# Kernel optimization log

Hardware: AMD Instinct MI355X
Metric: run time of the kernel (lower is better)

Reference implementation:

```python
import jax, jax.numpy as jnp
import numpy as np

NEG_SLOPE = 0.01  # torch nn.LeakyReLU default


def setup_inputs() -> dict:
    key = jax.random.key(0)
    kq, kk, kv, km, kw = jax.random.split(key, 5)
    B, Lq, Lk, Dk, Dv = 4, 2048, 2048, 512, 512
    q = jax.random.normal(kq, (B, Lq, Dk), dtype=jnp.float32)
    k = jax.random.normal(kk, (B, Lk, Dk), dtype=jnp.float32)
    v = jax.random.normal(kv, (B, Lk, Dv), dtype=jnp.float32)
    attn_mask = jax.random.randint(km, (B, Lq, Lk), 0, 2).astype(jnp.int32)
    # xavier_normal for (Dk, 1): std = sqrt(2 / (Dk + 1))
    weight = jax.random.normal(kw, (Dk, 1), dtype=jnp.float32) * np.sqrt(2.0 / (Dk + 1))
    return {"q": q, "k": k, "v": v, "attn_mask": attn_mask, "weight": weight}


def reference(q, k, v, attn_mask, weight):
    # (q - k) @ w  ==  (q @ w) - (k @ w): avoid the [B,Lq,Lk,Dk] intermediate.
    qw = jnp.einsum('bqd,do->bq', q, weight)  # [B, Lq]
    kw = jnp.einsum('bkd,do->bk', k, weight)  # [B, Lk]
    scores = qw[:, :, None] - kw[:, None, :]  # [B, Lq, Lk]
    attn = jnp.where(scores >= 0, scores, NEG_SLOPE * scores)  # LeakyReLU
    masked = attn_mask == 0
    attn = jnp.where(masked, -jnp.inf, attn)
    attn = jax.nn.softmax(attn, axis=2)
    attn = jnp.where(masked, 0.0, attn)
    # dropout omitted (eval mode / identity for reference correctness)
    output = jnp.einsum('bqk,bkd->bqd', attn, v)  # bmm
    return output, attn
```

## Files before the change

### kernel.cpp

```cpp
#include <hip/hip_runtime.h>
#include <math.h>

#define BB 4
#define LQ 2048
#define LK 2048
#define DK 512
#define DV 512

typedef __attribute__((ext_vector_type(8))) _Float16 f16x8;
typedef __attribute__((ext_vector_type(2))) _Float16 f16x2;
typedef __attribute__((ext_vector_type(4))) float f32x4;

#define WS_QW    0
#define WS_KW    8192
#define WS_M     16384
#define WS_INV   24576
#define WS_VF16  32768
#define NOUT     ((size_t)BB * LQ * DV)

__device__ __forceinline__ void lds_barrier() {
    __builtin_amdgcn_sched_barrier(0);
    asm volatile("s_waitcnt lgkmcnt(0)\n\ts_barrier" ::: "memory");
    __builtin_amdgcn_sched_barrier(0);
}

__global__ __launch_bounds__(256) void qkw_kernel(const float* __restrict__ q,
                                                  const float* __restrict__ k,
                                                  const float* __restrict__ w,
                                                  float* __restrict__ ws) {
    int gw   = (int)((blockIdx.x * blockDim.x + threadIdx.x) >> 6);
    int lane = threadIdx.x & 63;
    const int nq = BB * LQ;
    const float* row = (gw < nq) ? (q + (size_t)gw * DK) : (k + (size_t)(gw - nq) * DK);

    float acc = 0.f;
#pragma unroll
    for (int j = 0; j < DK; j += 256) {
        int idx = j + lane * 4;
        float4 rv = *reinterpret_cast<const float4*>(row + idx);
        float4 wv = *reinterpret_cast<const float4*>(w + idx);
        acc += rv.x * wv.x + rv.y * wv.y + rv.z * wv.z + rv.w * wv.w;
    }
#pragma unroll
    for (int off = 32; off >= 1; off >>= 1) acc += __shfl_xor(acc, off, 64);
    if (lane == 0) ws[gw] = acc;
}

__global__ __launch_bounds__(256) void vpack_kernel(const float* __restrict__ v,
                                                    unsigned short* __restrict__ vF) {
    __shared__ float tile[32][517];
    const int k32 = blockIdx.x;
    const int b   = blockIdx.y;
    const int k0  = k32 * 32;
    const int t   = threadIdx.x;

#pragma unroll
    for (int i = 0; i < 16; ++i) {
        int flat = i * 256 + t;
        int row  = flat >> 7;
        int c4   = flat & 127;
        float4 f = *reinterpret_cast<const float4*>(
            v + ((size_t)(b * LK + k0 + row)) * DV + c4 * 4);
        tile[row][c4 * 4 + 0] = f.x;
        tile[row][c4 * 4 + 1] = f.y;
        tile[row][c4 * 4 + 2] = f.z;
        tile[row][c4 * 4 + 3] = f.w;
    }
    __syncthreads();

    const int w = t >> 6, l = t & 63;
    const int rbase = (l >> 4) * 8;
#pragma unroll
    for (int f = 0; f < 8; ++f) {
        int n16 = w * 8 + f;
        int col = n16 * 16 + (l & 15);
        f16x8 vv;
#pragma unroll
        for (int j = 0; j < 8; ++j) vv[j] = (_Float16)tile[rbase + j][col];
        size_t u16base = (((size_t)(b * 32 + n16)) * 64 + k32) * 512;
        *reinterpret_cast<f16x8*>(vF + u16base + l * 8) = vv;
    }
}

__global__ __launch_bounds__(256) void rowstat_kernel(const int* __restrict__ mask,
                                                      float* __restrict__ ws,
                                                      float* __restrict__ attn) {
    __shared__ float kws[LK];
    const int b = (blockIdx.x * 4) / LQ;
    const int t = threadIdx.x;

    const float4* kw4 = reinterpret_cast<const float4*>(ws + WS_KW + b * LK);
#pragma unroll
    for (int i = 0; i < 2; ++i)
        reinterpret_cast<float4*>(kws)[t + i * 256] = kw4[t + i * 256];
    __syncthreads();

    const int wave = t >> 6, lane = t & 63;
    const int rid  = blockIdx.x * 4 + wave;
    const float qwv = ws[WS_QW + rid];
    const int* mrow = mask + (size_t)rid * LK;

    float m = -INFINITY, s = 0.f;
    unsigned int mybits = 0;
#pragma unroll
    for (int i = 0; i < 8; ++i) {
        int e = (i * 64 + lane) * 4;
        int4  mi = *reinterpret_cast<const int4*>(mrow + e);
        float4 kv = reinterpret_cast<const float4*>(kws)[i * 64 + lane];
        float vals[4] = {kv.x, kv.y, kv.z, kv.w};
        int   msks[4] = {mi.x, mi.y, mi.z, mi.w};

        unsigned int bits = (msks[0] ? 1u : 0u) | (msks[1] ? 2u : 0u) |
                            (msks[2] ? 4u : 0u) | (msks[3] ? 8u : 0u);
        mybits |= bits << (i * 4);

#pragma unroll
        for (int j = 0; j < 4; ++j) {
            float sc = qwv - vals[j];
            sc = fmaxf(sc, 0.01f * sc);
            if (msks[j]) {
                if (sc > m) { s = s * __expf(m - sc) + 1.f; m = sc; }
                else        { s += __expf(sc - m); }
            }
        }
    }
#pragma unroll
    for (int off = 32; off >= 1; off >>= 1) {
        float mo = __shfl_xor(m, off, 64);
        float so = __shfl_xor(s, off, 64);
        float M  = fmaxf(m, mo);
        float sa = (m  == M) ? s  : s  * __expf(m  - M);
        float sb = (mo == M) ? so : so * __expf(mo - M);
        m = M; s = sa + sb;
    }
    const float inv = (s > 0.f) ? 1.f / s : 0.f;
    if (lane == 0) {
        ws[WS_M   + rid] = m;
        ws[WS_INV + rid] = inv;
    }

    float* arow = attn + (size_t)rid * LK;
#pragma unroll
    for (int i = 0; i < 8; ++i) {
        float4 kv = reinterpret_cast<const float4*>(kws)[i * 64 + lane];
        float vals[4] = {kv.x, kv.y, kv.z, kv.w};
        unsigned int bits = (mybits >> (i * 4)) & 0xFu;
        float p[4];
#pragma unroll
        for (int j = 0; j < 4; ++j) {
            float sc = qwv - vals[j];
            sc = fmaxf(sc, 0.01f * sc);
            p[j] = (bits & (1u << j)) ? __expf(sc - m) * inv : 0.f;
        }
        *reinterpret_cast<float4*>(arow + (i * 64 + lane) * 4) =
            make_float4(p[0], p[1], p[2], p[3]);
    }
}

__global__ __launch_bounds__(256, 2) void pv_kernel(
        const float* __restrict__ attn,
        const unsigned short* __restrict__ vF,
        float* __restrict__ out) {
    __shared__ unsigned int pH32[2][1024];

    const int bid  = blockIdx.x;
    const int xcd  = bid & 7;
    const int rest = bid >> 3;
    const int g    = rest >> 2;
    const int ns   = rest & 3;
    const int qt4b = g * 8 + xcd;
    const int b    = qt4b & 3;
    const int qt   = qt4b >> 2;
    const int ksteps = LK >> 5;

    const int t = threadIdx.x;
    const int w = t >> 6, l = t & 63;

    const int row_a = (t >> 6) * 16 + (t & 15);
    const int kb    = ((t >> 4) & 3) * 8;
    const int rid   = b * LQ + qt * 64 + row_a;
    const float* arow = attn + (size_t)rid * LK + kb;

    const unsigned short* bsrc[2];
#pragma unroll
    for (int nb = 0; nb < 2; ++nb)
        bsrc[nb] = vF + (((size_t)(b * 32 + ns * 8 + w * 2 + nb)) * 64) * 512
                      + (size_t)l * 8;

    auto stage = [&](const float4& x, const float4& y, int buf) {
        unsigned int H[4];
        float f[8] = {x.x, x.y, x.z, x.w, y.x, y.y, y.z, y.w};
#pragma unroll
        for (int jw = 0; jw < 4; ++jw) {
            f16x2 hv;
            hv[0] = (_Float16)f[2 * jw];
            hv[1] = (_Float16)f[2 * jw + 1];
            H[jw] = __builtin_bit_cast(unsigned int, hv);
        }
        *reinterpret_cast<uint4*>(&pH32[buf][t * 4]) = *reinterpret_cast<uint4*>(H);
    };

    f16x8 bC[2], bN[2];
#pragma unroll
    for (int nb = 0; nb < 2; ++nb)
        bC[nb] = *reinterpret_cast<const f16x8*>(bsrc[nb]);

    {
        float4 x = *reinterpret_cast<const float4*>(arow);
        float4 y = *reinterpret_cast<const float4*>(arow + 4);
        stage(x, y, 0);
    }
    float4 aCx = *reinterpret_cast<const float4*>(arow + 32);
    float4 aCy = *reinterpret_cast<const float4*>(arow + 36);

    f32x4 acc[4][2];
#pragma unroll
    for (int mf = 0; mf < 4; ++mf)
#pragma unroll
        for (int nb = 0; nb < 2; ++nb)
            acc[mf][nb] = (f32x4){0.f, 0.f, 0.f, 0.f};

    lds_barrier();

    for (int s = 0; s < ksteps; ++s) {
        const int buf  = s & 1;
        const int nbuf = buf ^ 1;
        const int sn   = (s + 1 < ksteps) ? s + 1 : s;
        const int sn2  = (s + 2 < ksteps) ? s + 2 : s;

#pragma unroll
        for (int nb = 0; nb < 2; ++nb)
            bN[nb] = *reinterpret_cast<const f16x8*>(bsrc[nb] + (size_t)sn * 512);
        float4 aNx = *reinterpret_cast<const float4*>(arow + sn2 * 32);
        float4 aNy = *reinterpret_cast<const float4*>(arow + sn2 * 32 + 4);

        stage(aCx, aCy, nbuf);

        const f16x8* pHf = reinterpret_cast<const f16x8*>(pH32[buf]);
        f16x8 aH[4];
#pragma unroll
        for (int mf = 0; mf < 4; ++mf)
            aH[mf] = pHf[mf * 64 + l];

        __builtin_amdgcn_s_setprio(1);
#pragma unroll
        for (int nb = 0; nb < 2; ++nb)
#pragma unroll
            for (int mf = 0; mf < 4; ++mf)
                acc[mf][nb] = __builtin_amdgcn_mfma_f32_16x16x32_f16(aH[mf], bC[nb], acc[mf][nb], 0, 0, 0);
        __builtin_amdgcn_s_setprio(0);

        lds_barrier();

#pragma unroll
        for (int nb = 0; nb < 2; ++nb) bC[nb] = bN[nb];
        aCx = aNx; aCy = aNy;
    }

    float* obase = out + ((size_t)(b * LQ + qt * 64)) * DV
                       + ns * 128 + w * 32 + (l & 15);
#pragma unroll
    for (int mf = 0; mf < 4; ++mf)
#pragma unroll
        for (int nb = 0; nb < 2; ++nb)
#pragma unroll
            for (int r = 0; r < 4; ++r)
                obase[(size_t)(mf * 16 + (l >> 4) * 4 + r) * DV + nb * 16] = acc[mf][nb][r];
}

extern "C" void kernel_launch(void* const* d_in, const int* in_sizes, int n_in,
                              void* d_out, int out_size, void* d_ws, size_t ws_size,
                              hipStream_t stream) {
    const float* q    = (const float*)d_in[0];
    const float* k    = (const float*)d_in[1];
    const float* v    = (const float*)d_in[2];
    const int*   mask = (const int*)d_in[3];
    const float* w    = (const float*)d_in[4];

    float* out  = (float*)d_out;
    float* attn = out + NOUT;
    float* ws   = (float*)d_ws;

    unsigned short* vF = (unsigned short*)(ws + WS_VF16);

    qkw_kernel<<<4096, 256, 0, stream>>>(q, k, w, ws);
    vpack_kernel<<<dim3(64, 4), 256, 0, stream>>>(v, vF);
    rowstat_kernel<<<2048, 256, 0, stream>>>(mask, ws, attn);
    pv_kernel<<<512, 256, 0, stream>>>(attn, vF, out);
}
```

Measured before the change: 79.57 us.

## Fuse attention probability computation into PV kernel using packed mask bits

The row-statistics kernel now stores only max, inverse sum and a bit-packed mask instead of writing the full probability matrix. The PV kernel recomputes probabilities from qw, kw and the row statistics, writes attn from one of the four column-split blocks, and feeds fp16 copies to the MFMA. This removes a full fp32 read of the attention matrix from global memory. In exchange it adds exp recomputation in every column block and uneven store work across blocks.

Measured after the change: 105.6 us. +32.7%, slower.

```diff
diff --git a/kernel.cpp b/kernel.cpp
--- a/kernel.cpp
+++ b/kernel.cpp
@@ -15,7 +15,8 @@
 #define WS_KW    8192
 #define WS_M     16384
 #define WS_INV   24576
-#define WS_VF16  32768
+#define WS_MPACK 32768
+#define WS_VF16  557056
 #define NOUT     ((size_t)BB * LQ * DV)
 
 __device__ __forceinline__ void lds_barrier() {
@@ -82,9 +83,9 @@
     }
 }
 
-__global__ __launch_bounds__(256) void rowstat_kernel(const int* __restrict__ mask,
+__global__ __launch_bounds__(256) void prestat_kernel(const int* __restrict__ mask,
                                                       float* __restrict__ ws,
-                                                      float* __restrict__ attn) {
+                                                      unsigned int* __restrict__ mpack) {
     __shared__ float kws[LK];
     const int b = (blockIdx.x * 4) / LQ;
     const int t = threadIdx.x;
@@ -101,7 +102,6 @@
     const int* mrow = mask + (size_t)rid * LK;
 
     float m = -INFINITY, s = 0.f;
-    unsigned int mybits = 0;
 #pragma unroll
     for (int i = 0; i < 8; ++i) {
         int e = (i * 64 + lane) * 4;
@@ -112,7 +112,11 @@
 
         unsigned int bits = (msks[0] ? 1u : 0u) | (msks[1] ? 2u : 0u) |
                             (msks[2] ? 4u : 0u) | (msks[3] ? 8u : 0u);
-        mybits |= bits << (i * 4);
+        unsigned int wv = bits << ((lane & 7) * 4);
+        wv |= __shfl_xor(wv, 1, 64);
+        wv |= __shfl_xor(wv, 2, 64);
+        wv |= __shfl_xor(wv, 4, 64);
+        if ((lane & 7) == 0) mpack[(size_t)rid * 64 + i * 8 + (lane >> 3)] = wv;
 
 #pragma unroll
         for (int j = 0; j < 4; ++j) {
@@ -133,34 +137,19 @@
         float sb = (mo == M) ? so : so * __expf(mo - M);
         m = M; s = sa + sb;
     }
-    const float inv = (s > 0.f) ? 1.f / s : 0.f;
     if (lane == 0) {
         ws[WS_M   + rid] = m;
-        ws[WS_INV + rid] = inv;
-    }
-
-    float* arow = attn + (size_t)rid * LK;
-#pragma unroll
-    for (int i = 0; i < 8; ++i) {
-        float4 kv = reinterpret_cast<const float4*>(kws)[i * 64 + lane];
-        float vals[4] = {kv.x, kv.y, kv.z, kv.w};
-        unsigned int bits = (mybits >> (i * 4)) & 0xFu;
-        float p[4];
-#pragma unroll
-        for (int j = 0; j < 4; ++j) {
-            float sc = qwv - vals[j];
-            sc = fmaxf(sc, 0.01f * sc);
-            p[j] = (bits & (1u << j)) ? __expf(sc - m) * inv : 0.f;
-        }
-        *reinterpret_cast<float4*>(arow + (i * 64 + lane) * 4) =
-            make_float4(p[0], p[1], p[2], p[3]);
+        ws[WS_INV + rid] = (s > 0.f) ? 1.f / s : 0.f;
     }
 }
 
 __global__ __launch_bounds__(256, 2) void pv_kernel(
-        const float* __restrict__ attn,
+        const unsigned int* __restrict__ mpack,
+        const float* __restrict__ ws,
         const unsigned short* __restrict__ vF,
+        float* __restrict__ attn,
         float* __restrict__ out) {
+    __shared__ float kw_lds[LK];
     __shared__ unsigned int pH32[2][1024];
 
     const int bid  = blockIdx.x;
@@ -179,7 +168,16 @@
     const int row_a = (t >> 6) * 16 + (t & 15);
     const int kb    = ((t >> 4) & 3) * 8;
     const int rid   = b * LQ + qt * 64 + row_a;
-    const float* arow = attn + (size_t)rid * LK + kb;
+
+    for (int i = t; i < LK; i += 256)
+        kw_lds[i] = ws[WS_KW + b * LK + i];
+
+    const float qv = ws[WS_QW  + rid];
+    const float mv = ws[WS_M   + rid];
+    const float iv = ws[WS_INV + rid];
+    const unsigned int* mrow = mpack + (size_t)rid * 64;
+    float* arow = attn + (size_t)rid * LK + kb;
+    const bool write_attn = (ns == 0);
 
     const unsigned short* bsrc[2];
 #pragma unroll
@@ -187,14 +185,27 @@
         bsrc[nb] = vF + (((size_t)(b * 32 + ns * 8 + w * 2 + nb)) * 64) * 512
                       + (size_t)l * 8;
 
-    auto stage = [&](const float4& x, const float4& y, int buf) {
+    auto compute_p = [&](int s, int buf) {
+        const unsigned int mw = mrow[s];
+        float p[8];
+#pragma unroll
+        for (int i = 0; i < 8; ++i) {
+            float sc = qv - kw_lds[s * 32 + kb + i];
+            sc = fmaxf(sc, 0.01f * sc);
+            p[i] = ((mw >> (kb + i)) & 1u) ? __expf(sc - mv) * iv : 0.f;
+        }
+        if (write_attn) {
+            *reinterpret_cast<float4*>(arow + s * 32) =
+                make_float4(p[0], p[1], p[2], p[3]);
+            *reinterpret_cast<float4*>(arow + s * 32 + 4) =
+                make_float4(p[4], p[5], p[6], p[7]);
+        }
         unsigned int H[4];
-        float f[8] = {x.x, x.y, x.z, x.w, y.x, y.y, y.z, y.w};
 #pragma unroll
         for (int jw = 0; jw < 4; ++jw) {
             f16x2 hv;
-            hv[0] = (_Float16)f[2 * jw];
-            hv[1] = (_Float16)f[2 * jw + 1];
+            hv[0] = (_Float16)p[2 * jw];
+            hv[1] = (_Float16)p[2 * jw + 1];
             H[jw] = __builtin_bit_cast(unsigned int, hv);
         }
         *reinterpret_cast<uint4*>(&pH32[buf][t * 4]) = *reinterpret_cast<uint4*>(H);
@@ -205,13 +216,8 @@
     for (int nb = 0; nb < 2; ++nb)
         bC[nb] = *reinterpret_cast<const f16x8*>(bsrc[nb]);
 
-    {
-        float4 x = *reinterpret_cast<const float4*>(arow);
-        float4 y = *reinterpret_cast<const float4*>(arow + 4);
-        stage(x, y, 0);
-    }
-    float4 aCx = *reinterpret_cast<const float4*>(arow + 32);
-    float4 aCy = *reinterpret_cast<const float4*>(arow + 36);
+    lds_barrier();
+    compute_p(0, 0);
 
     f32x4 acc[4][2];
 #pragma unroll
@@ -226,15 +232,12 @@
         const int buf  = s & 1;
         const int nbuf = buf ^ 1;
         const int sn   = (s + 1 < ksteps) ? s + 1 : s;
-        const int sn2  = (s + 2 < ksteps) ? s + 2 : s;
 
 #pragma unroll
         for (int nb = 0; nb < 2; ++nb)
             bN[nb] = *reinterpret_cast<const f16x8*>(bsrc[nb] + (size_t)sn * 512);
-        float4 aNx = *reinterpret_cast<const float4*>(arow + sn2 * 32);
-        float4 aNy = *reinterpret_cast<const float4*>(arow + sn2 * 32 + 4);
-
-        stage(aCx, aCy, nbuf);
+
+        compute_p(sn, nbuf);
 
         const f16x8* pHf = reinterpret_cast<const f16x8*>(pH32[buf]);
         f16x8 aH[4];
@@ -254,7 +257,6 @@
 
 #pragma unroll
         for (int nb = 0; nb < 2; ++nb) bC[nb] = bN[nb];
-        aCx = aNx; aCy = aNy;
     }
 
     float* obase = out + ((size_t)(b * LQ + qt * 64)) * DV
@@ -281,10 +283,11 @@
     float* attn = out + NOUT;
     float* ws   = (float*)d_ws;
 
-    unsigned short* vF = (unsigned short*)(ws + WS_VF16);
+    unsigned int*   mpack = (unsigned int*)(ws + WS_MPACK);
+    unsigned short* vF    = (unsigned short*)(ws + WS_VF16);
 
     qkw_kernel<<<4096, 256, 0, stream>>>(q, k, w, ws);
     vpack_kernel<<<dim3(64, 4), 256, 0, stream>>>(v, vF);
-    rowstat_kernel<<<2048, 256, 0, stream>>>(mask, ws, attn);
-    pv_kernel<<<512, 256, 0, stream>>>(attn, vF, out);
-}
+    prestat_kernel<<<2048, 256, 0, stream>>>(mask, ws, mpack);
+    pv_kernel<<<512, 256, 0, stream>>>(mpack, ws, vF, attn, out);
+}
```
